# Kernel optimization log

Hardware: AMD Instinct MI355X
Metric: run time of the kernel (lower is better)

## Reference

```python
import jax, jax.numpy as jnp
import numpy as np


def setup_inputs() -> dict:
    key = jax.random.key(0)
    k0, k1, k2, k3 = jax.random.split(key, 4)
    B, T, M, E, H = 4, 2048, 1024, 8, 4096
    x = jax.random.normal(k0, (B, T, M), dtype=jnp.float32)
    wg = jax.random.normal(k1, (M, E), dtype=jnp.float32) * 0.02
    w1 = jax.random.normal(k2, (E, M, H), dtype=jnp.float32) * 0.02
    w2 = jax.random.normal(k3, (E, H, M), dtype=jnp.float32) * 0.02
    return {"x": x, "wg": wg, "w1": w1, "w2": w2}


def reference(x, wg, w1, w2):
    """GShard MoE layer: top-1 gate + dense one-hot dispatch/combine + expert FFN."""
    M = x.shape[-1]
    xs = x.reshape(-1, M)                      # [s, m]
    s = xs.shape[0]
    E = wg.shape[1]
    capacity = s // E                          # capacity_factor = 1.0

    # ---- top-1 gate (deepspeed/gshard top1gating) ----
    logits = xs @ wg                           # [s, e]
    gates = jax.nn.softmax(logits, axis=-1)
    idx = jnp.argmax(gates, axis=1)            # [s]
    mask1 = jax.nn.one_hot(idx, E, dtype=gates.dtype)  # [s, e]
    me = gates.mean(axis=0)
    ce = mask1.mean(axis=0)
    l_aux = jnp.sum(me * ce) * E
    # position of each token within its expert's buffer
    locations = jnp.cumsum(mask1, axis=0) - 1.0          # [s, e]
    mask1 = mask1 * (locations < capacity).astype(gates.dtype)  # drop overflow
    gates1 = gates * mask1                                 # [s, e]
    loc_s = jnp.sum(locations * mask1, axis=1).astype(jnp.int32)  # [s]
    loc_sc = jax.nn.one_hot(loc_s, capacity, dtype=gates.dtype)   # [s, c]
    combine = gates1[:, :, None] * loc_sc[:, None, :]       # [s, e, c]
    dispatch = (combine > 0).astype(x.dtype)                # [s, e, c]

    # ---- dense one-hot dispatch (the kernel-headroom hotspot) ----
    dispatched = jnp.einsum('sec,sm->ecm', dispatch, xs)    # [e, c, m]

    # ---- per-expert 2-layer FFN ----
    h = jax.nn.relu(jnp.einsum('ecm,emh->ech', dispatched, w1))
    expert_out = jnp.einsum('ech,ehm->ecm', h, w2)          # [e, c, m]

    # ---- dense one-hot combine ----
    out = jnp.einsum('sec,ecm->sm', combine, expert_out).reshape(x.shape)
    return out, l_aux
```

## Files before the change

kernel.cpp:

```cpp
#include <hip/hip_runtime.h>
#include <hip/hip_bf16.h>

#define S_TOK 8192
#define MDIM  1024
#define EXP   8
#define HDIM  4096
#define CAP   1024

typedef __attribute__((ext_vector_type(8))) short short8;
typedef __attribute__((ext_vector_type(4))) float floatx4;

#define BARRIER() asm volatile("s_barrier" ::: "memory")
#define WAITV6()  asm volatile("s_waitcnt vmcnt(6)" ::: "memory")
#define WAITV0()  asm volatile("s_waitcnt vmcnt(0)" ::: "memory")
#define SCHEDB()  __builtin_amdgcn_sched_barrier(0)

__device__ __forceinline__ unsigned short f2b(float f) {
    union { float f; unsigned int i; } v; v.f = f;
    unsigned int r = v.i + 0x7fffu + ((v.i >> 16) & 1u);
    return (unsigned short)(r >> 16);
}

__device__ __forceinline__ void gl2lds16(const unsigned short* g, unsigned short* l) {
    __builtin_amdgcn_global_load_lds(
        (const __attribute__((address_space(1))) unsigned int*)g,
        (__attribute__((address_space(3))) unsigned int*)l,
        16, 0, 0);
}

__global__ __launch_bounds__(256) void gate_kernel(
    const float* __restrict__ x, const float* __restrict__ wg,
    float* __restrict__ gates8, int* __restrict__ token_expert,
    unsigned short* __restrict__ xb16)
{
    const int wave = threadIdx.x >> 6, lane = threadIdx.x & 63;
    const int s = blockIdx.x * 4 + wave;

    const float* xr = x + (size_t)s * MDIM + lane * 16;
    float xv[16];
#pragma unroll
    for (int q = 0; q < 4; ++q) *(float4*)(xv + q * 4) = *(const float4*)(xr + q * 4);

    if (xb16) {
        unsigned short bv[16];
#pragma unroll
        for (int j = 0; j < 16; ++j) bv[j] = f2b(xv[j]);
        int4* dst = (int4*)(xb16 + (size_t)s * MDIM + lane * 16);
        dst[0] = ((const int4*)bv)[0];
        dst[1] = ((const int4*)bv)[1];
    }

    float acc[EXP];
#pragma unroll
    for (int e = 0; e < EXP; ++e) acc[e] = 0.f;
    const int m0 = lane * 16;
#pragma unroll
    for (int j = 0; j < 16; ++j) {
        const float xm = xv[j];
        const float* wr = wg + (size_t)(m0 + j) * EXP;
        float4 w0 = *(const float4*)(wr);
        float4 w1v = *(const float4*)(wr + 4);
        acc[0] += xm * w0.x; acc[1] += xm * w0.y; acc[2] += xm * w0.z; acc[3] += xm * w0.w;
        acc[4] += xm * w1v.x; acc[5] += xm * w1v.y; acc[6] += xm * w1v.z; acc[7] += xm * w1v.w;
    }
#pragma unroll
    for (int e = 0; e < EXP; ++e) {
#pragma unroll
        for (int off = 32; off > 0; off >>= 1)
            acc[e] += __shfl_down(acc[e], off);
    }
    if (lane == 0) {
        float mx = acc[0]; int idx = 0;
#pragma unroll
        for (int e = 1; e < EXP; ++e) if (acc[e] > mx) { mx = acc[e]; idx = e; }
        float g[EXP]; float sum = 0.f;
#pragma unroll
        for (int e = 0; e < EXP; ++e) { g[e] = expf(acc[e] - mx); sum += g[e]; }
        float inv = 1.f / sum;
#pragma unroll
        for (int e = 0; e < EXP; ++e) gates8[(size_t)s * EXP + e] = g[e] * inv;
        token_expert[s] = idx;
    }
}

__device__ __forceinline__ void transpose_tile(
    const float* __restrict__ src, unsigned short* __restrict__ dst,
    int R, int C, int R0, int C0, unsigned short* Ls)
{
    const int t = threadIdx.x;
    {
        const int r = t >> 2, c0 = (t & 3) * 16;
        const float* p = src + (size_t)(R0 + r) * C + C0 + c0;
        float f[16];
#pragma unroll
        for (int q = 0; q < 4; ++q) *(float4*)(f + q * 4) = ((const float4*)p)[q];
#pragma unroll
        for (int j = 0; j < 16; ++j) Ls[(c0 + j) * 72 + r] = f2b(f[j]);
    }
    __syncthreads();
    {
        const int c = t >> 2, m0 = (t & 3) * 16;
        int4 v0 = *(const int4*)&Ls[c * 72 + m0];
        int4 v1 = *(const int4*)&Ls[c * 72 + m0 + 8];
        int4* q = (int4*)(dst + (size_t)(C0 + c) * R + R0 + m0);
        q[0] = v0; q[1] = v1;
    }
}

__global__ __launch_bounds__(256) void mega_prep(
    const float* __restrict__ gates8, const int* __restrict__ token_expert,
    int* __restrict__ slot_token, float* __restrict__ slot_gate,
    float* __restrict__ laux_out,
    const float* __restrict__ w1, const float* __restrict__ w2,
    unsigned short* __restrict__ W1T, unsigned short* __restrict__ W2T,
    float* __restrict__ outz)
{
    __shared__ int            cntS[256 * EXP];
    __shared__ float          fsumS[256 * EXP];
    __shared__ unsigned short Ls[64 * 72];

    const int b = blockIdx.x;
    const int t = threadIdx.x;

    if (b == 0) {
        for (int i = t; i < EXP * CAP; i += 256) slot_token[i] = -1;

        int local[EXP];
#pragma unroll
        for (int e = 0; e < EXP; ++e) local[e] = 0;
        const int s0 = t * 32;
        for (int j = 0; j < 32; ++j) local[token_expert[s0 + j]]++;

        int incl[EXP];
#pragma unroll
        for (int e = 0; e < EXP; ++e) { incl[e] = local[e]; cntS[t * EXP + e] = incl[e]; }
        __syncthreads();
        for (int d = 1; d < 256; d <<= 1) {
            int add[EXP];
            if (t >= d) {
#pragma unroll
                for (int e = 0; e < EXP; ++e) add[e] = cntS[(t - d) * EXP + e];
            }
            __syncthreads();
            if (t >= d) {
#pragma unroll
                for (int e = 0; e < EXP; ++e) { incl[e] += add[e]; cntS[t * EXP + e] = incl[e]; }
            }
            __syncthreads();
        }

        int off[EXP];
#pragma unroll
        for (int e = 0; e < EXP; ++e) off[e] = incl[e] - local[e];
        for (int j = 0; j < 32; ++j) {
            int s = s0 + j;
            int e = token_expert[s];
            int loc = off[e]++;
            if (loc < CAP) {
                int slot = e * CAP + loc;
                slot_token[slot] = s;
                slot_gate[slot]  = gates8[(size_t)s * EXP + e];
            }
        }

        float ms[EXP];
#pragma unroll
        for (int e = 0; e < EXP; ++e) ms[e] = 0.f;
        for (int j = 0; j < 32; ++j) {
            const float* g = gates8 + (size_t)(s0 + j) * EXP;
#pragma unroll
            for (int e = 0; e < EXP; ++e) ms[e] += g[e];
        }
#pragma unroll
        for (int e = 0; e < EXP; ++e) fsumS[t * EXP + e] = ms[e];
        __syncthreads();
        for (int st = 128; st > 0; st >>= 1) {
            if (t < st) {
#pragma unroll
                for (int e = 0; e < EXP; ++e) fsumS[t * EXP + e] += fsumS[(t + st) * EXP + e];
            }
            __syncthreads();
        }
        if (t == 0) {
            float l = 0.f;
#pragma unroll
            for (int e = 0; e < EXP; ++e)
                l += (fsumS[e] / (float)S_TOK) * ((float)cntS[255 * EXP + e] / (float)S_TOK);
            laux_out[0] = l * (float)EXP;
        }
        return;
    }

    if (b <= 2048) {
        float4* p = (float4*)(outz + (size_t)(b - 1) * 4096 + t * 16);
        const float4 z = {0.f, 0.f, 0.f, 0.f};
        p[0] = z; p[1] = z; p[2] = z; p[3] = z;
        return;
    }

    int i = b - 2049;
    if (i < 8192) {
        const int e = i >> 10, rem = i & 1023;
        const int bx = rem & 63, by = rem >> 6;
        transpose_tile(w1 + (size_t)e * MDIM * HDIM, W1T + (size_t)e * MDIM * HDIM,
                       MDIM, HDIM, by * 64, bx * 64, Ls);
        return;
    }
    i -= 8192;
    {
        const int e = i >> 10, rem = i & 1023;
        const int bx = rem & 15, by = rem >> 4;
        transpose_tile(w2 + (size_t)e * MDIM * HDIM, W2T + (size_t)e * MDIM * HDIM,
                       HDIM, MDIM, by * 64, bx * 64, Ls);
    }
}

__global__ __launch_bounds__(256) void transpose_cvt(
    const float* __restrict__ src, unsigned short* __restrict__ dst, int R, int C)
{
    __shared__ unsigned short Ls[64 * 72];
    const size_t eo = (size_t)blockIdx.z * R * C;
    transpose_tile(src + eo, dst + eo, R, C, blockIdx.y * 64, blockIdx.x * 64, Ls);
}

template<int KT, int N, bool SCATTER, bool GATHER>
__global__ __launch_bounds__(512, 2) void ffn_gemm_8p(
    const unsigned short* __restrict__ Ag, const unsigned short* __restrict__ BT,
    void* __restrict__ Outv,
    const int* __restrict__ slot_token, const float* __restrict__ slot_gate)
{
    constexpr int K   = KT * 64;
    constexpr int NBX = N / 128;
    constexpr int NWG = NBX * (CAP / 256);

    extern __shared__ __align__(16) unsigned short sm[];
    unsigned short* Abuf = sm;
    unsigned short* Bbuf = sm + 3 * 16384;

    const int e    = blockIdx.z;
    const int orig = blockIdx.x;
    const int logical = (orig & 7) * (NWG >> 3) + (orig >> 3);
    const int nb = (logical % NBX) * 128;
    const int ib = (logical / NBX) * 256;

    const int tid  = threadIdx.x;
    const int lane = tid & 63, wave = tid >> 6;
    const int quad = lane >> 4, l15 = lane & 15;
    const int wm = wave >> 2, wn = wave & 3;

    const int rr   = tid >> 3;
    const int slot = (tid & 7) ^ (rr & 7);

    const unsigned short* sA0;
    const unsigned short* sA1;
    const unsigned short* sA2;
    const unsigned short* sA3;
    if (GATHER) {
        const int base = e * CAP + ib + rr;
        int t0 = slot_token[base];
        int t1 = slot_token[base + 64];
        int t2 = slot_token[base + 128];
        int t3 = slot_token[base + 192];
        sA0 = Ag + (size_t)(t0 < 0 ? 0 : t0) * K + slot * 8;
        sA1 = Ag + (size_t)(t1 < 0 ? 0 : t1) * K + slot * 8;
        sA2 = Ag + (size_t)(t2 < 0 ? 0 : t2) * K + slot * 8;
        sA3 = Ag + (size_t)(t3 < 0 ? 0 : t3) * K + slot * 8;
    } else {
        sA0 = Ag + (size_t)(e * CAP + ib + rr) * K + slot * 8;
        sA1 = sA0 + (size_t)64 * K;
        sA2 = sA0 + (size_t)128 * K;
        sA3 = sA0 + (size_t)192 * K;
    }
    const unsigned short* Bsrc = BT + ((size_t)e * N + nb + rr) * K + slot * 8;

    auto stageA = [&](int buf, int t, const unsigned short* s, int ca) {
        gl2lds16(s + t * 64, Abuf + buf * 16384 + ca * 4096 + wave * 512);
    };
    auto stageB = [&](int buf, int t, int cb) {
        gl2lds16(Bsrc + (size_t)cb * 64 * K + t * 64,
                 Bbuf + buf * 8192 + cb * 4096 + wave * 512);
    };

    const int sx  = l15 & 7;
    const int ko0 = ((0 + quad) ^ sx) * 8;
    const int ko1 = ((4 + quad) ^ sx) * 8;
    const int arow = wm * 128 + l15;
    const int brow = wn * 32 + l15;

    floatx4 acc[8][2];
#pragma unroll
    for (int i = 0; i < 8; ++i)
#pragma unroll
        for (int j = 0; j < 2; ++j)
            acc[i][j] = (floatx4){0.f, 0.f, 0.f, 0.f};

    stageA(0, 0, sA0, 0); stageA(0, 0, sA1, 1); stageA(0, 0, sA2, 2); stageA(0, 0, sA3, 3);
    stageB(0, 0, 0); stageB(0, 0, 1);
    stageA(1, 1, sA0, 0); stageA(1, 1, sA1, 1); stageA(1, 1, sA2, 2); stageA(1, 1, sA3, 3);
    stageB(1, 1, 0); stageB(1, 1, 1);
    WAITV6();
    BARRIER();

    int buf = 0;
    for (int t = 0; t < KT; ++t) {
        const int nbuf = (buf >= 1) ? buf - 1 : 2;
        const bool st  = (t + 2 < KT);

        short8 brg[2][2];
#pragma unroll
        for (int fn = 0; fn < 2; ++fn) {
            const int row = brow + fn * 16;
            brg[fn][0] = *(const short8*)&Bbuf[buf * 8192 + row * 64 + ko0];
            brg[fn][1] = *(const short8*)&Bbuf[buf * 8192 + row * 64 + ko1];
        }
        short8 aA[8];
#pragma unroll
        for (int fm = 0; fm < 4; ++fm) {
            const int row = arow + fm * 16;
            aA[fm * 2 + 0] = *(const short8*)&Abuf[buf * 16384 + row * 64 + ko0];
            aA[fm * 2 + 1] = *(const short8*)&Abuf[buf * 16384 + row * 64 + ko1];
        }
        if (st) { stageA(nbuf, t + 2, sA0, 0); stageA(nbuf, t + 2, sA1, 1); }
        BARRIER(); SCHEDB();
        __builtin_amdgcn_s_setprio(1);
#pragma unroll
        for (int fm = 0; fm < 4; ++fm) {
            acc[fm][0] = __builtin_amdgcn_mfma_f32_16x16x32_bf16(aA[fm*2+0], brg[0][0], acc[fm][0], 0, 0, 0);
            acc[fm][0] = __builtin_amdgcn_mfma_f32_16x16x32_bf16(aA[fm*2+1], brg[0][1], acc[fm][0], 0, 0, 0);
        }
        __builtin_amdgcn_s_setprio(0); SCHEDB(); BARRIER();

        short8 aB[8];
#pragma unroll
        for (int fm = 0; fm < 4; ++fm) {
            const int row = arow + 64 + fm * 16;
            aB[fm * 2 + 0] = *(const short8*)&Abuf[buf * 16384 + row * 64 + ko0];
            aB[fm * 2 + 1] = *(const short8*)&Abuf[buf * 16384 + row * 64 + ko1];
        }
        if (st) { stageA(nbuf, t + 2, sA2, 2); stageA(nbuf, t + 2, sA3, 3); }
        BARRIER(); SCHEDB();
        __builtin_amdgcn_s_setprio(1);
#pragma unroll
        for (int fm = 0; fm < 4; ++fm) {
            acc[fm][1] = __builtin_amdgcn_mfma_f32_16x16x32_bf16(aA[fm*2+0], brg[1][0], acc[fm][1], 0, 0, 0);
            acc[fm][1] = __builtin_amdgcn_mfma_f32_16x16x32_bf16(aA[fm*2+1], brg[1][1], acc[fm][1], 0, 0, 0);
        }
        __builtin_amdgcn_s_setprio(0); SCHEDB(); BARRIER();

        if (st) stageB(nbuf, t + 2, 0);
        BARRIER(); SCHEDB();
        __builtin_amdgcn_s_setprio(1);
#pragma unroll
        for (int fm = 0; fm < 4; ++fm) {
            acc[4+fm][0] = __builtin_amdgcn_mfma_f32_16x16x32_bf16(aB[fm*2+0], brg[0][0], acc[4+fm][0], 0, 0, 0);
            acc[4+fm][0] = __builtin_amdgcn_mfma_f32_16x16x32_bf16(aB[fm*2+1], brg[0][1], acc[4+fm][0], 0, 0, 0);
        }
        __builtin_amdgcn_s_setprio(0); SCHEDB(); BARRIER();

        if (st) stageB(nbuf, t + 2, 1);
        BARRIER(); SCHEDB();
        __builtin_amdgcn_s_setprio(1);
#pragma unroll
        for (int fm = 0; fm < 4; ++fm) {
            acc[4+fm][1] = __builtin_amdgcn_mfma_f32_16x16x32_bf16(aB[fm*2+0], brg[1][0], acc[4+fm][1], 0, 0, 0);
            acc[4+fm][1] = __builtin_amdgcn_mfma_f32_16x16x32_bf16(aB[fm*2+1], brg[1][1], acc[4+fm][1], 0, 0, 0);
        }
        __builtin_amdgcn_s_setprio(0); SCHEDB();
        if (t + 1 < KT) {
            if (st) WAITV6(); else WAITV0();
            BARRIER();
        }
        buf = (buf == 2) ? 0 : buf + 1;
    }

#pragma unroll
    for (int FM = 0; FM < 8; ++FM) {
        const int rowb = ib + wm * 128 + FM * 16 + quad * 4;
#pragma unroll
        for (int r = 0; r < 4; ++r) {
            const int gi = rowb + r;
            if (SCATTER) {
                const int slotI = e * CAP + gi;
                const int tok = slot_token[slotI];
                if (tok >= 0) {
                    const float gsc = slot_gate[slotI];
                    float* Out = (float*)Outv;
#pragma unroll
                    for (int fn = 0; fn < 2; ++fn) {
                        const int gn = nb + wn * 32 + fn * 16 + l15;
                        Out[(size_t)tok * N + gn] = gsc * acc[FM][fn][r];
                    }
                }
            } else {
                unsigned short* Out = (unsigned short*)Outv;
#pragma unroll
                for (int fn = 0; fn < 2; ++fn) {
                    const int gn = nb + wn * 32 + fn * 16 + l15;
                    Out[((size_t)e * CAP + gi) * N + gn] = f2b(fmaxf(acc[FM][fn][r], 0.f));
                }
            }
        }
    }
}

__global__ __launch_bounds__(256) void scan_kernel(
    const float* __restrict__ gates8, const int* __restrict__ token_expert,
    int* __restrict__ slot_token, float* __restrict__ slot_gate,
    float* __restrict__ laux_out)
{
    __shared__ int   cnt[256][EXP];
    __shared__ float fsum[256][EXP];
    __shared__ int   tot[EXP];
    const int t = threadIdx.x;

    for (int i = t; i < EXP * CAP; i += 256) slot_token[i] = -1;

    int local[EXP];
#pragma unroll
    for (int e = 0; e < EXP; ++e) local[e] = 0;
    const int s0 = t * 32;
    for (int j = 0; j < 32; ++j) local[token_expert[s0 + j]]++;
#pragma unroll
    for (int e = 0; e < EXP; ++e) cnt[t][e] = local[e];
    __syncthreads();

    if (t < EXP) {
        int run = 0;
        for (int i = 0; i < 256; ++i) { int v = cnt[i][t]; cnt[i][t] = run; run += v; }
        tot[t] = run;
    }
    __syncthreads();

    int off[EXP];
#pragma unroll
    for (int e = 0; e < EXP; ++e) off[e] = cnt[t][e];
    for (int j = 0; j < 32; ++j) {
        int s = s0 + j;
        int e = token_expert[s];
        int loc = off[e]++;
        if (loc < CAP) {
            int slot = e * CAP + loc;
            slot_token[slot] = s;
            slot_gate[slot]  = gates8[(size_t)s * EXP + e];
        }
    }

    float ms[EXP];
#pragma unroll
    for (int e = 0; e < EXP; ++e) ms[e] = 0.f;
    for (int j = 0; j < 32; ++j) {
        const float* g = gates8 + (size_t)(s0 + j) * EXP;
#pragma unroll
        for (int e = 0; e < EXP; ++e) ms[e] += g[e];
    }
#pragma unroll
    for (int e = 0; e < EXP; ++e) fsum[t][e] = ms[e];
    __syncthreads();
    for (int st = 128; st > 0; st >>= 1) {
        if (t < st) {
#pragma unroll
            for (int e = 0; e < EXP; ++e) fsum[t][e] += fsum[t + st][e];
        }
        __syncthreads();
    }
    if (t == 0) {
        float l = 0.f;
#pragma unroll
        for (int e = 0; e < EXP; ++e)
            l += (fsum[0][e] / (float)S_TOK) * ((float)tot[e] / (float)S_TOK);
        laux_out[0] = l * (float)EXP;
    }
}

template<int KSTEPS, int N, bool GATHER, bool SCATTER>
__global__ __launch_bounds__(256) void ffn_gemm_slow(
    const void* __restrict__ Agv, const float* __restrict__ Bg,
    void* __restrict__ Outv,
    const int* __restrict__ slot_token, const float* __restrict__ slot_gate)
{
    constexpr int K = KSTEPS * 32;
    const int e  = blockIdx.z;
    const int ib = blockIdx.y * 128;
    const int nb = blockIdx.x * 128;
    const int t  = threadIdx.x;

    __shared__ unsigned short As[128 * 40];
    __shared__ unsigned short Bs[32 * 136];

    const float* B = Bg + (size_t)e * K * N;
    const int arow  = t >> 1;
    const int ahalf = t & 1;
    const float* ArowF = nullptr;
    const unsigned short* ArowH = nullptr;
    bool avalid = true;
    if (GATHER) {
        int tok = slot_token[e * CAP + ib + arow];
        avalid = (tok >= 0);
        ArowF = (const float*)Agv + (size_t)(avalid ? tok : 0) * K;
    } else {
        ArowH = (const unsigned short*)Agv + ((size_t)e * CAP + ib + arow) * K;
    }
    const int bk  = t >> 3;
    const int bn0 = (t & 7) * 16;
    const float* Bptr = B + (size_t)bk * N + nb + bn0;

    const int lane = t & 63, wave = t >> 6;
    const int quad = lane >> 4, l15 = lane & 15;
    const int wr = wave >> 1, wc = wave & 1;

    floatx4 acc[4][4];
#pragma unroll
    for (int r = 0; r < 4; ++r)
#pragma unroll
        for (int c = 0; c < 4; ++c)
            acc[r][c] = (floatx4){0.f, 0.f, 0.f, 0.f};

    for (int kb = 0; kb < KSTEPS; ++kb) {
        const int k0 = kb * 32;
        unsigned short av[16];
        if (GATHER) {
            if (avalid) {
                const float4* p = (const float4*)(ArowF + k0 + ahalf * 16);
                float4 f0 = p[0], f1 = p[1], f2 = p[2], f3 = p[3];
                const float fa[16] = {f0.x,f0.y,f0.z,f0.w, f1.x,f1.y,f1.z,f1.w,
                                      f2.x,f2.y,f2.z,f2.w, f3.x,f3.y,f3.z,f3.w};
#pragma unroll
                for (int j = 0; j < 16; ++j) av[j] = f2b(fa[j]);
            } else {
#pragma unroll
                for (int j = 0; j < 16; ++j) av[j] = 0;
            }
        } else {
            const int4* p = (const int4*)(ArowH + k0 + ahalf * 16);
            *(int4*)(av)     = p[0];
            *(int4*)(av + 8) = p[1];
        }
        unsigned short bv[16];
        {
            const float4* q = (const float4*)(Bptr + (size_t)k0 * N);
            float4 f0 = q[0], f1 = q[1], f2 = q[2], f3 = q[3];
            const float fb[16] = {f0.x,f0.y,f0.z,f0.w, f1.x,f1.y,f1.z,f1.w,
                                  f2.x,f2.y,f2.z,f2.w, f3.x,f3.y,f3.z,f3.w};
#pragma unroll
            for (int j = 0; j < 16; ++j) bv[j] = f2b(fb[j]);
        }

        *(int4*)&As[arow * 40 + ahalf * 16]     = *(int4*)(av);
        *(int4*)&As[arow * 40 + ahalf * 16 + 8] = *(int4*)(av + 8);
        *(int4*)&Bs[bk * 136 + bn0]             = *(int4*)(bv);
        *(int4*)&Bs[bk * 136 + bn0 + 8]         = *(int4*)(bv + 8);
        __syncthreads();

        short8 af[4];
#pragma unroll
        for (int r = 0; r < 4; ++r)
            af[r] = *(const short8*)&As[(wr * 64 + r * 16 + l15) * 40 + quad * 8];
        short8 bfr[4];
#pragma unroll
        for (int c = 0; c < 4; ++c) {
#pragma unroll
            for (int j = 0; j < 8; ++j)
                bfr[c][j] = (short)Bs[(quad * 8 + j) * 136 + wc * 64 + c * 16 + l15];
        }
#pragma unroll
        for (int r = 0; r < 4; ++r)
#pragma unroll
            for (int c = 0; c < 4; ++c)
                acc[r][c] = __builtin_amdgcn_mfma_f32_16x16x32_bf16(af[r], bfr[c], acc[r][c], 0, 0, 0);
        __syncthreads();
    }

#pragma unroll
    for (int r = 0; r < 4; ++r) {
#pragma unroll
        for (int reg = 0; reg < 4; ++reg) {
            const int gi = ib + wr * 64 + r * 16 + quad * 4 + reg;
            if (SCATTER) {
                const int slot = e * CAP + gi;
                const int tok = slot_token[slot];
                if (tok >= 0) {
                    const float gsc = slot_gate[slot];
                    float* Out = (float*)Outv;
#pragma unroll
                    for (int c = 0; c < 4; ++c) {
                        const int gn = nb + wc * 64 + c * 16 + l15;
                        Out[(size_t)tok * N + gn] = gsc * acc[r][c][reg];
                    }
                }
            } else {
                unsigned short* Out = (unsigned short*)Outv;
#pragma unroll
                for (int c = 0; c < 4; ++c) {
                    const int gn = nb + wc * 64 + c * 16 + l15;
                    Out[((size_t)e * CAP + gi) * N + gn] = f2b(fmaxf(acc[r][c][reg], 0.f));
                }
            }
        }
    }
}

extern "C" void kernel_launch(void* const* d_in, const int* in_sizes, int n_in,
                              void* d_out, int out_size, void* d_ws, size_t ws_size,
                              hipStream_t stream)
{
    const float* x  = (const float*)d_in[0];
    const float* wg = (const float*)d_in[1];
    const float* w1 = (const float*)d_in[2];
    const float* w2 = (const float*)d_in[3];
    float* out = (float*)d_out;
    float* laux = out + (size_t)S_TOK * MDIM;

    char* ws = (char*)d_ws;
    float* gates8       = (float*)(ws);
    int*   token_expert = (int*)(ws + 262144);
    int*   slot_token   = (int*)(ws + 294912);
    float* slot_gate    = (float*)(ws + 327680);
    unsigned short* xb16 = (unsigned short*)(ws + 360448);
    unsigned short* h    = (unsigned short*)(ws + 17137664);
    unsigned short* W1T  = (unsigned short*)(ws + 84246528);
    unsigned short* W2T  = (unsigned short*)(ws + 151355392);

    const size_t FAST_NEED = 151355392ull;
    const size_t WIDE_NEED = 218464256ull;

    if (ws_size >= FAST_NEED) {
        const bool wide = (ws_size >= WIDE_NEED);

        static bool tried = false, ok8 = false;
        if (!tried) {
            tried = true;
            ok8 = (hipFuncSetAttribute((const void*)ffn_gemm_8p<16, HDIM, false, true>,
                       hipFuncAttributeMaxDynamicSharedMemorySize, 147456) == hipSuccess)
               && (hipFuncSetAttribute((const void*)ffn_gemm_8p<64, MDIM, true, false>,
                       hipFuncAttributeMaxDynamicSharedMemorySize, 147456) == hipSuccess);
        }

        gate_kernel<<<dim3(S_TOK / 4), dim3(256), 0, stream>>>(x, wg, gates8, token_expert, xb16);

        const int nblk = 1 + 2048 + 8192 + (wide ? 8192 : 0);
        mega_prep<<<dim3(nblk), dim3(256), 0, stream>>>(
            gates8, token_expert, slot_token, slot_gate, laux,
            w1, w2, W1T, wide ? W2T : W1T, out);

        if (ok8) {
            ffn_gemm_8p<16, HDIM, false, true><<<dim3((HDIM/128)*(CAP/256), 1, EXP), dim3(512), 147456, stream>>>(
                xb16, W1T, h, slot_token, slot_gate);
            if (!wide)
                transpose_cvt<<<dim3(MDIM / 64, HDIM / 64, EXP), dim3(256), 0, stream>>>(w2, W1T, HDIM, MDIM);
            ffn_gemm_8p<64, MDIM, true, false><<<dim3((MDIM/128)*(CAP/256), 1, EXP), dim3(512), 147456, stream>>>(
                h, wide ? W2T : W1T, out, slot_token, slot_gate);
        } else {
            ffn_gemm_slow<32, HDIM, true, false><<<dim3(HDIM / 128, CAP / 128, EXP), dim3(256), 0, stream>>>(
                x, w1, h, slot_token, slot_gate);
            ffn_gemm_slow<128, MDIM, false, true><<<dim3(MDIM / 128, CAP / 128, EXP), dim3(256), 0, stream>>>(
                h, w2, out, slot_token, slot_gate);
        }
    } else {
        hipMemsetAsync(d_out, 0, (size_t)out_size * 4, stream);
        gate_kernel<<<dim3(S_TOK / 4), dim3(256), 0, stream>>>(x, wg, gates8, token_expert, nullptr);
        scan_kernel<<<dim3(1), dim3(256), 0, stream>>>(gates8, token_expert, slot_token, slot_gate, laux);
        unsigned short* hs = (unsigned short*)(ws + 360448);
        ffn_gemm_slow<32, HDIM, true, false><<<dim3(HDIM / 128, CAP / 128, EXP), dim3(256), 0, stream>>>(
            x, w1, hs, slot_token, slot_gate);
        ffn_gemm_slow<128, MDIM, false, true><<<dim3(MDIM / 128, CAP / 128, EXP), dim3(256), 0, stream>>>(
            hs, w2, out, slot_token, slot_gate);
    }
}
```

Before: 549.4 us.

## Fuse w1 transpose into gate kernel, register-tile transposes, merge GEMM phases

Moves the w1 fp32→bf16 transpose out of the prep kernel and into the gate kernel as extra blocks, so the two independent jobs share one launch. All transposes now work on 64x256 tiles held in registers, each thread transposing an 8x8 block, instead of bouncing 64x64 tiles through LDS with a barrier. The GEMM main loop also merges four MFMA phases into two, issuing all A stages and then both B stages together, which halves the barriers per k-step. The risks are higher register pressure, narrower 16-byte strided stores in the transpose, and less interleaving of loads with MFMAs. The fallback path now passes xb16 and h pointers into the fused gate kernel, and that may be unsafe when the workspace is small.

```diff
diff --git a/kernel.cpp b/kernel.cpp
--- a/kernel.cpp
+++ b/kernel.cpp
@@ -28,20 +28,55 @@
         16, 0, 0);
 }
 
-__global__ __launch_bounds__(256) void gate_kernel(
+__device__ __forceinline__ void transpose_tile_reg(
+    const float* __restrict__ src, unsigned short* __restrict__ dst,
+    int R, int C, int R0, int C0)
+{
+    const int t  = threadIdx.x;
+    const int rg = t & 7;
+    const int cg = t >> 3;
+    const float* p = src + (size_t)(R0 + rg * 8) * C + C0 + cg * 8;
+    float v[8][8];
+#pragma unroll
+    for (int i = 0; i < 8; ++i) {
+        *(float4*)&v[i][0] = *(const float4*)(p + (size_t)i * C);
+        *(float4*)&v[i][4] = *(const float4*)(p + (size_t)i * C + 4);
+    }
+    unsigned short* q = dst + (size_t)(C0 + cg * 8) * R + R0 + rg * 8;
+#pragma unroll
+    for (int j = 0; j < 8; ++j) {
+        unsigned short o[8];
+#pragma unroll
+        for (int i = 0; i < 8; ++i) o[i] = f2b(v[i][j]);
+        *(int4*)(q + (size_t)j * R) = *(const int4*)o;
+    }
+}
+
+__global__ __launch_bounds__(256) void gate_fused(
     const float* __restrict__ x, const float* __restrict__ wg,
     float* __restrict__ gates8, int* __restrict__ token_expert,
-    unsigned short* __restrict__ xb16)
-{
+    unsigned short* __restrict__ xb16,
+    const float* __restrict__ w1, unsigned short* __restrict__ W1T)
+{
+    const int b = blockIdx.x;
+    if (b >= 2048) {
+        const int i = b - 2048;
+        const int e = i >> 8, rem = i & 255;
+        const int bx = rem & 15, by = rem >> 4;
+        transpose_tile_reg(w1 + (size_t)e * MDIM * HDIM, W1T + (size_t)e * MDIM * HDIM,
+                           MDIM, HDIM, by * 64, bx * 256);
+        return;
+    }
+
     const int wave = threadIdx.x >> 6, lane = threadIdx.x & 63;
-    const int s = blockIdx.x * 4 + wave;
+    const int s = b * 4 + wave;
 
     const float* xr = x + (size_t)s * MDIM + lane * 16;
     float xv[16];
 #pragma unroll
     for (int q = 0; q < 4; ++q) *(float4*)(xv + q * 4) = *(const float4*)(xr + q * 4);
 
-    if (xb16) {
+    {
         unsigned short bv[16];
 #pragma unroll
         for (int j = 0; j < 16; ++j) bv[j] = f2b(xv[j]);
@@ -83,41 +118,15 @@
     }
 }
 
-__device__ __forceinline__ void transpose_tile(
-    const float* __restrict__ src, unsigned short* __restrict__ dst,
-    int R, int C, int R0, int C0, unsigned short* Ls)
-{
-    const int t = threadIdx.x;
-    {
-        const int r = t >> 2, c0 = (t & 3) * 16;
-        const float* p = src + (size_t)(R0 + r) * C + C0 + c0;
-        float f[16];
-#pragma unroll
-        for (int q = 0; q < 4; ++q) *(float4*)(f + q * 4) = ((const float4*)p)[q];
-#pragma unroll
-        for (int j = 0; j < 16; ++j) Ls[(c0 + j) * 72 + r] = f2b(f[j]);
-    }
-    __syncthreads();
-    {
-        const int c = t >> 2, m0 = (t & 3) * 16;
-        int4 v0 = *(const int4*)&Ls[c * 72 + m0];
-        int4 v1 = *(const int4*)&Ls[c * 72 + m0 + 8];
-        int4* q = (int4*)(dst + (size_t)(C0 + c) * R + R0 + m0);
-        q[0] = v0; q[1] = v1;
-    }
-}
-
 __global__ __launch_bounds__(256) void mega_prep(
     const float* __restrict__ gates8, const int* __restrict__ token_expert,
     int* __restrict__ slot_token, float* __restrict__ slot_gate,
     float* __restrict__ laux_out,
-    const float* __restrict__ w1, const float* __restrict__ w2,
-    unsigned short* __restrict__ W1T, unsigned short* __restrict__ W2T,
+    const float* __restrict__ w2, unsigned short* __restrict__ W2T,
     float* __restrict__ outz)
 {
-    __shared__ int            cntS[256 * EXP];
-    __shared__ float          fsumS[256 * EXP];
-    __shared__ unsigned short Ls[64 * 72];
+    __shared__ int   cntS[256 * EXP];
+    __shared__ float fsumS[256 * EXP];
 
     const int b = blockIdx.x;
     const int t = threadIdx.x;
@@ -198,29 +207,22 @@
         return;
     }
 
-    int i = b - 2049;
-    if (i < 8192) {
-        const int e = i >> 10, rem = i & 1023;
-        const int bx = rem & 63, by = rem >> 6;
-        transpose_tile(w1 + (size_t)e * MDIM * HDIM, W1T + (size_t)e * MDIM * HDIM,
-                       MDIM, HDIM, by * 64, bx * 64, Ls);
-        return;
-    }
-    i -= 8192;
-    {
-        const int e = i >> 10, rem = i & 1023;
-        const int bx = rem & 15, by = rem >> 4;
-        transpose_tile(w2 + (size_t)e * MDIM * HDIM, W2T + (size_t)e * MDIM * HDIM,
-                       HDIM, MDIM, by * 64, bx * 64, Ls);
-    }
-}
-
-__global__ __launch_bounds__(256) void transpose_cvt(
-    const float* __restrict__ src, unsigned short* __restrict__ dst, int R, int C)
-{
-    __shared__ unsigned short Ls[64 * 72];
-    const size_t eo = (size_t)blockIdx.z * R * C;
-    transpose_tile(src + eo, dst + eo, R, C, blockIdx.y * 64, blockIdx.x * 64, Ls);
+    const int i = b - 2049;
+    const int e = i >> 8, rem = i & 255;
+    const int bx = rem & 3, by = rem >> 2;
+    transpose_tile_reg(w2 + (size_t)e * MDIM * HDIM, W2T + (size_t)e * MDIM * HDIM,
+                       HDIM, MDIM, by * 64, bx * 256);
+}
+
+__global__ __launch_bounds__(256) void transpose_reg(
+    const float* __restrict__ src, unsigned short* __restrict__ dst,
+    int R, int C, int ct)
+{
+    const int i = blockIdx.x;
+    const int e = i >> 8, rem = i & 255;
+    const int bx = rem % ct, by = rem / ct;
+    transpose_tile_reg(src + (size_t)e * R * C, dst + (size_t)e * R * C,
+                       R, C, by * 64, bx * 256);
 }
 
 template<int KT, int N, bool SCATTER, bool GATHER>
@@ -320,13 +322,18 @@
             aA[fm * 2 + 0] = *(const short8*)&Abuf[buf * 16384 + row * 64 + ko0];
             aA[fm * 2 + 1] = *(const short8*)&Abuf[buf * 16384 + row * 64 + ko1];
         }
-        if (st) { stageA(nbuf, t + 2, sA0, 0); stageA(nbuf, t + 2, sA1, 1); }
+        if (st) {
+            stageA(nbuf, t + 2, sA0, 0); stageA(nbuf, t + 2, sA1, 1);
+            stageA(nbuf, t + 2, sA2, 2); stageA(nbuf, t + 2, sA3, 3);
+        }
         BARRIER(); SCHEDB();
         __builtin_amdgcn_s_setprio(1);
 #pragma unroll
         for (int fm = 0; fm < 4; ++fm) {
             acc[fm][0] = __builtin_amdgcn_mfma_f32_16x16x32_bf16(aA[fm*2+0], brg[0][0], acc[fm][0], 0, 0, 0);
             acc[fm][0] = __builtin_amdgcn_mfma_f32_16x16x32_bf16(aA[fm*2+1], brg[0][1], acc[fm][0], 0, 0, 0);
+            acc[fm][1] = __builtin_amdgcn_mfma_f32_16x16x32_bf16(aA[fm*2+0], brg[1][0], acc[fm][1], 0, 0, 0);
+            acc[fm][1] = __builtin_amdgcn_mfma_f32_16x16x32_bf16(aA[fm*2+1], brg[1][1], acc[fm][1], 0, 0, 0);
         }
         __builtin_amdgcn_s_setprio(0); SCHEDB(); BARRIER();
 
@@ -337,31 +344,13 @@
             aB[fm * 2 + 0] = *(const short8*)&Abuf[buf * 16384 + row * 64 + ko0];
             aB[fm * 2 + 1] = *(const short8*)&Abuf[buf * 16384 + row * 64 + ko1];
         }
-        if (st) { stageA(nbuf, t + 2, sA2, 2); stageA(nbuf, t + 2, sA3, 3); }
-        BARRIER(); SCHEDB();
-        __builtin_amdgcn_s_setprio(1);
-#pragma unroll
-        for (int fm = 0; fm < 4; ++fm) {
-            acc[fm][1] = __builtin_amdgcn_mfma_f32_16x16x32_bf16(aA[fm*2+0], brg[1][0], acc[fm][1], 0, 0, 0);
-            acc[fm][1] = __builtin_amdgcn_mfma_f32_16x16x32_bf16(aA[fm*2+1], brg[1][1], acc[fm][1], 0, 0, 0);
-        }
-        __builtin_amdgcn_s_setprio(0); SCHEDB(); BARRIER();
-
-        if (st) stageB(nbuf, t + 2, 0);
+        if (st) { stageB(nbuf, t + 2, 0); stageB(nbuf, t + 2, 1); }
         BARRIER(); SCHEDB();
         __builtin_amdgcn_s_setprio(1);
 #pragma unroll
         for (int fm = 0; fm < 4; ++fm) {
             acc[4+fm][0] = __builtin_amdgcn_mfma_f32_16x16x32_bf16(aB[fm*2+0], brg[0][0], acc[4+fm][0], 0, 0, 0);
             acc[4+fm][0] = __builtin_amdgcn_mfma_f32_16x16x32_bf16(aB[fm*2+1], brg[0][1], acc[4+fm][0], 0, 0, 0);
-        }
-        __builtin_amdgcn_s_setprio(0); SCHEDB(); BARRIER();
-
-        if (st) stageB(nbuf, t + 2, 1);
-        BARRIER(); SCHEDB();
-        __builtin_amdgcn_s_setprio(1);
-#pragma unroll
-        for (int fm = 0; fm < 4; ++fm) {
             acc[4+fm][1] = __builtin_amdgcn_mfma_f32_16x16x32_bf16(aB[fm*2+0], brg[1][0], acc[4+fm][1], 0, 0, 0);
             acc[4+fm][1] = __builtin_amdgcn_mfma_f32_16x16x32_bf16(aB[fm*2+1], brg[1][1], acc[4+fm][1], 0, 0, 0);
         }
@@ -635,18 +624,19 @@
                        hipFuncAttributeMaxDynamicSharedMemorySize, 147456) == hipSuccess);
         }
 
-        gate_kernel<<<dim3(S_TOK / 4), dim3(256), 0, stream>>>(x, wg, gates8, token_expert, xb16);
-
-        const int nblk = 1 + 2048 + 8192 + (wide ? 8192 : 0);
+        gate_fused<<<dim3(4096), dim3(256), 0, stream>>>(
+            x, wg, gates8, token_expert, xb16, w1, W1T);
+
+        const int nblk = 1 + 2048 + (wide ? 2048 : 0);
         mega_prep<<<dim3(nblk), dim3(256), 0, stream>>>(
             gates8, token_expert, slot_token, slot_gate, laux,
-            w1, w2, W1T, wide ? W2T : W1T, out);
+            w2, wide ? W2T : W1T, out);
 
         if (ok8) {
             ffn_gemm_8p<16, HDIM, false, true><<<dim3((HDIM/128)*(CAP/256), 1, EXP), dim3(512), 147456, stream>>>(
                 xb16, W1T, h, slot_token, slot_gate);
             if (!wide)
-                transpose_cvt<<<dim3(MDIM / 64, HDIM / 64, EXP), dim3(256), 0, stream>>>(w2, W1T, HDIM, MDIM);
+                transpose_reg<<<dim3(2048), dim3(256), 0, stream>>>(w2, W1T, HDIM, MDIM, MDIM / 256);
             ffn_gemm_8p<64, MDIM, true, false><<<dim3((MDIM/128)*(CAP/256), 1, EXP), dim3(512), 147456, stream>>>(
                 h, wide ? W2T : W1T, out, slot_token, slot_gate);
         } else {
@@ -657,7 +647,8 @@
         }
     } else {
         hipMemsetAsync(d_out, 0, (size_t)out_size * 4, stream);
-        gate_kernel<<<dim3(S_TOK / 4), dim3(256), 0, stream>>>(x, wg, gates8, token_expert, nullptr);
+        gate_fused<<<dim3(2048), dim3(256), 0, stream>>>(
+            x, wg, gates8, token_expert, xb16, w1, (unsigned short*)h);
         scan_kernel<<<dim3(1), dim3(256), 0, stream>>>(gates8, token_expert, slot_token, slot_gate, laux);
         unsigned short* hs = (unsigned short*)(ws + 360448);
         ffn_gemm_slow<32, HDIM, true, false><<<dim3(HDIM / 128, CAP / 128, EXP), dim3(256), 0, stream>>>(
```

Result: slower. 566.8 us (+3.2%).
